# Kernel tuning notes

Measured on AMD Instinct MI355X. Metric: run time of the kernel, lower is better.

## Reference

```python
import jax, jax.numpy as jnp
import numpy as np

N, E = 50000, 400000
H, C = 2, 128          # heads, embedding_size
HC = H * C
HID = 256              # hidden_size
TARGET = 1234
NEG_SLOPE = 0.2


def gatv2_conv(x, src, dst, edge_attr, Wl, bl, Wr, br, We, att, b_out):
    """PyG GATv2Conv, concat=True, share_weights=False, edge_dim given."""
    n = x.shape[0]
    xl = (x @ Wl + bl).reshape(n, H, C)   # lin_l -> source side
    xr = (x @ Wr + br).reshape(n, H, C)   # lin_r -> target side
    e = (edge_attr @ We).reshape(-1, H, C)  # lin_edge (no bias)
    m = xl[src] + xr[dst] + e             # [E,H,C]
    s = jax.nn.leaky_relu(m, NEG_SLOPE)
    alpha = jnp.einsum('ehc,hc->eh', s, att)  # [E,H]
    # segment softmax over destination nodes
    amax = jax.ops.segment_max(alpha, dst, num_segments=n)
    amax = jnp.where(jnp.isfinite(amax), amax, 0.0)
    ex = jnp.exp(alpha - amax[dst])
    den = jax.ops.segment_sum(ex, dst, num_segments=n)
    a = ex / (den[dst] + 1e-16)
    msg = (xl[src] * a[:, :, None]).reshape(-1, HC)
    out = jax.ops.segment_sum(msg, dst, num_segments=n)
    return out + b_out                    # [N, H*C]


def setup_inputs() -> dict:
    key = jax.random.key(0)
    ks = jax.random.split(key, 20)
    g = lambda k, shp, s=0.1: (jax.random.normal(k, shp, dtype=jnp.float32) * s)
    inp = {
        'x': jax.random.normal(ks[0], (N, 2), dtype=jnp.float32),
        'edge_index': jax.random.randint(ks[1], (2, E), 0, N, dtype=jnp.int32),
        'edge_attr': jax.random.uniform(ks[2], (E, 1), dtype=jnp.float32),
        'labels': jnp.zeros((N,), dtype=jnp.int32).at[TARGET].set(1),
        # conv1 params (in=2)
        'Wl1': g(ks[3], (2, HC)), 'bl1': jnp.zeros((HC,), jnp.float32),
        'Wr1': g(ks[4], (2, HC)), 'br1': jnp.zeros((HC,), jnp.float32),
        'We1': g(ks[5], (1, HC)), 'att1': g(ks[6], (H, C)),
        'bo1': jnp.zeros((HC,), jnp.float32),
        # conv2 params (lazy in_channels inferred as 2, since it is fed x)
        'Wl2': g(ks[7], (2, HC)), 'bl2': jnp.zeros((HC,), jnp.float32),
        'Wr2': g(ks[8], (2, HC)), 'br2': jnp.zeros((HC,), jnp.float32),
        'We2': g(ks[9], (1, HC)), 'att2': g(ks[10], (H, C)),
        'bo2': jnp.zeros((HC,), jnp.float32),
        # fc
        'Wfc': g(ks[11], (HC, HID)), 'bfc': jnp.zeros((HID,), jnp.float32),
    }
    return inp


def reference(x, edge_index, edge_attr, labels,
              Wl1, bl1, Wr1, br1, We1, att1, bo1,
              Wl2, bl2, Wr2, br2, We2, att2, bo2,
              Wfc, bfc):
    src, dst = edge_index[0], edge_index[1]
    # conv1 (computed as in source; its output is overwritten by conv2(x))
    h1 = jax.nn.relu(gatv2_conv(x, src, dst, edge_attr, Wl1, bl1, Wr1, br1, We1, att1, bo1))
    h = jax.nn.relu(gatv2_conv(x, src, dst, edge_attr, Wl2, bl2, Wr2, br2, We2, att2, bo2))
    target_idx = jnp.argmax(labels)
    te = h[target_idx][None, :]           # [1, H*C]
    out = te @ Wfc + bfc                  # [1, hidden]
    return out
```

## Files before the change

kernel.cpp:

```cpp
#include <hip/hip_runtime.h>
#include <stdint.h>


#define MAXE 512
#define NEG_SLOPE 0.2f
#define HC 256
#define FCBLOCKS 8

struct Ws {
    unsigned long long key;
    int count;
    int pad;
    int list[MAXE];
};

__device__ __forceinline__ unsigned long long enc_key(int val, int idx) {
    return ((unsigned long long)(~(((unsigned)val) ^ 0x80000000u)) << 32)
           | (unsigned long long)(unsigned)idx;
}

__global__ void argmax_zero_kernel(const int* __restrict__ labels, int n,
                                   Ws* __restrict__ ws, float* __restrict__ out) {
    __shared__ unsigned long long sred[256];
    const int tid = threadIdx.x;
    int t = blockIdx.x * blockDim.x + tid;
    unsigned long long best = ~0ull;
    int i0 = t * 4;
    if (i0 + 3 < n) {
        int4 v = *reinterpret_cast<const int4*>(labels + i0);
        int vals[4] = {v.x, v.y, v.z, v.w};
        #pragma unroll
        for (int j = 0; j < 4; ++j) {
            unsigned long long key = enc_key(vals[j], i0 + j);
            if (key < best) best = key;
        }
    } else {
        for (int j = 0; j < 4; ++j) {
            int i = i0 + j;
            if (i < n) {
                unsigned long long key = enc_key(labels[i], i);
                if (key < best) best = key;
            }
        }
    }
    sred[tid] = best;
    __syncthreads();
    for (int off = 128; off > 0; off >>= 1) {
        if (tid < off) {
            if (sred[tid + off] < sred[tid]) sred[tid] = sred[tid + off];
        }
        __syncthreads();
    }
    if (tid == 0) atomicMin(&ws->key, sred[0]);
    if (blockIdx.x == 0) {
        if (tid == 0) ws->count = 0;
        out[tid] = 0.f;
    }
}

__device__ __forceinline__ int decode_target(const Ws* ws) {
    return (int)(unsigned)(ws->key & 0xFFFFFFFFull);
}

__global__ void filter_kernel(const int* __restrict__ dstArr, int E,
                              Ws* __restrict__ ws) {
    const int target = decode_target(ws);
    int t = blockIdx.x * blockDim.x + threadIdx.x;
    int i0 = t * 4;
    if (i0 + 3 < E) {
        int4 v = *reinterpret_cast<const int4*>(dstArr + i0);
        int vals[4] = {v.x, v.y, v.z, v.w};
        #pragma unroll
        for (int j = 0; j < 4; ++j) {
            if (vals[j] == target) {
                int pos = atomicAdd(&ws->count, 1);
                if (pos < MAXE) ws->list[pos] = i0 + j;
            }
        }
    } else {
        for (int j = 0; j < 4; ++j) {
            int i = i0 + j;
            if (i < E && dstArr[i] == target) {
                int pos = atomicAdd(&ws->count, 1);
                if (pos < MAXE) ws->list[pos] = i;
            }
        }
    }
}

__global__ void gat_fc_kernel(const float* __restrict__ x,
                              const int* __restrict__ srcArr,
                              const float* __restrict__ edge_attr,
                              const float* __restrict__ Wl, const float* __restrict__ bl,
                              const float* __restrict__ Wr, const float* __restrict__ br,
                              const float* __restrict__ We, const float* __restrict__ att,
                              const float* __restrict__ bo,
                              const float* __restrict__ Wfc, const float* __restrict__ bfc,
                              const Ws* __restrict__ ws,
                              float* __restrict__ out) {
    const int tid = threadIdx.x;
    const int h = tid >> 7;

    __shared__ float sx0[MAXE], sx1[MAXE], sea[MAXE];
    __shared__ float salpha[2 * MAXE];
    __shared__ float wred[4];
    __shared__ float te_s[HC];

    const int target = decode_target(ws);
    int K = ws->count;
    if (K > MAXE) K = MAXE;

    const float xt0 = x[2 * target], xt1 = x[2 * target + 1];
    const float wl0 = Wl[tid], wl1 = Wl[HC + tid], blv = bl[tid];
    const float xr  = xt0 * Wr[tid] + xt1 * Wr[HC + tid] + br[tid];
    const float wev = We[tid];
    const float attv = att[tid];

    for (int base = 0; base < K; base += 256) {
        int k = base + tid;
        if (k < K) {
            int e = ws->list[k];
            int s = srcArr[e];
            sx0[k] = x[2 * s];
            sx1[k] = x[2 * s + 1];
            sea[k] = edge_attr[e];
        }
    }
    __syncthreads();

    for (int k = 0; k < K; ++k) {
        float xl = sx0[k] * wl0 + sx1[k] * wl1 + blv;
        float m = xl + xr + sea[k] * wev;
        float sl = (m >= 0.f) ? m : NEG_SLOPE * m;
        float v = sl * attv;
        #pragma unroll
        for (int off = 32; off > 0; off >>= 1) v += __shfl_down(v, off, 64);
        if ((tid & 63) == 0) wred[tid >> 6] = v;
        __syncthreads();
        if (tid == 0) {
            salpha[2 * k]     = wred[0] + wred[1];
            salpha[2 * k + 1] = wred[2] + wred[3];
        }
        __syncthreads();
    }

    float amax = -3.0e38f;
    for (int k = 0; k < K; ++k) amax = fmaxf(amax, salpha[2 * k + h]);
    float den = 0.f;
    for (int k = 0; k < K; ++k) den += expf(salpha[2 * k + h] - amax);
    float inv = 1.f / (den + 1e-16f);

    float msg = 0.f;
    for (int k = 0; k < K; ++k) {
        float xl = sx0[k] * wl0 + sx1[k] * wl1 + blv;
        msg += expf(salpha[2 * k + h] - amax) * inv * xl;
    }
    float tv = msg + bo[tid];
    te_s[tid] = tv > 0.f ? tv : 0.f;
    __syncthreads();

    float acc = (blockIdx.x == 0) ? bfc[tid] : 0.f;
    const int r0 = blockIdx.x * (HC / FCBLOCKS);
    #pragma unroll
    for (int r = 0; r < HC / FCBLOCKS; ++r)
        acc += te_s[r0 + r] * Wfc[(r0 + r) * HC + tid];
    atomicAdd(&out[tid], acc);
}

extern "C" void kernel_launch(void* const* d_in, const int* in_sizes, int n_in,
                              void* d_out, int out_size, void* d_ws, size_t ws_size,
                              hipStream_t stream) {
    const float* x          = (const float*)d_in[0];
    const int*   edge_index = (const int*)  d_in[1];
    const float* edge_attr  = (const float*)d_in[2];
    const int*   labels     = (const int*)  d_in[3];
    const float* Wl2  = (const float*)d_in[11];
    const float* bl2  = (const float*)d_in[12];
    const float* Wr2  = (const float*)d_in[13];
    const float* br2  = (const float*)d_in[14];
    const float* We2  = (const float*)d_in[15];
    const float* att2 = (const float*)d_in[16];
    const float* bo2  = (const float*)d_in[17];
    const float* Wfc  = (const float*)d_in[18];
    const float* bfc  = (const float*)d_in[19];

    const int N = in_sizes[3];
    const int E = in_sizes[1] / 2;
    const int* srcArr = edge_index;
    const int* dstArr = edge_index + E;

    Ws* ws = (Ws*)d_ws;
    float* out = (float*)d_out;

    int n4 = (N + 3) / 4;
    argmax_zero_kernel<<<(n4 + 255) / 256, 256, 0, stream>>>(labels, N, ws, out);

    int e4 = (E + 3) / 4;
    filter_kernel<<<(e4 + 255) / 256, 256, 0, stream>>>(dstArr, E, ws);

    gat_fc_kernel<<<FCBLOCKS, 256, 0, stream>>>(x, srcArr, edge_attr,
                                                Wl2, bl2, Wr2, br2, We2, att2, bo2,
                                                Wfc, bfc, ws, out);
}
```

Baseline: 102.8 us.

## Fuse argmax, edge filter and GAT/FC into one persistent kernel with grid barriers

Replaces the three launches (label argmax, destination-edge filter, attention plus FC) with a single 96-block kernel. Stages are separated by atomic-counter grid barriers with spin-sleep. Each thread prefetches its dst int4 chunks before waiting on the first barrier, and the FC weight rows are loaded into registers early to hide latency. The first barrier assumes the workspace counter starts at a fixed poison value, and the spin barriers assume all blocks are co-resident.

```diff
diff --git a/kernel.cpp b/kernel.cpp
--- a/kernel.cpp
+++ b/kernel.cpp
@@ -2,13 +2,19 @@
 #include <stdint.h>
 
 
+#define GRID 96
+#define FCB  32
+#define ROWS (256 / FCB)
 #define MAXE 512
 #define NEG_SLOPE 0.2f
 #define HC 256
-#define FCBLOCKS 8
+#define EPT 8
+#define POIS32 0xAAAAAAAAu
 
 struct Ws {
     unsigned long long key;
+    unsigned int done1;
+    unsigned int done2;
     int count;
     int pad;
     int list[MAXE];
@@ -19,112 +25,146 @@
            | (unsigned long long)(unsigned)idx;
 }
 
-__global__ void argmax_zero_kernel(const int* __restrict__ labels, int n,
-                                   Ws* __restrict__ ws, float* __restrict__ out) {
+__global__ void __launch_bounds__(256) fused_kernel(
+    const float* __restrict__ x,
+    const int* __restrict__ srcArr, const int* __restrict__ dstArr,
+    const float* __restrict__ edge_attr, const int* __restrict__ labels,
+    int N, int E,
+    const float* __restrict__ Wl, const float* __restrict__ bl,
+    const float* __restrict__ Wr, const float* __restrict__ br,
+    const float* __restrict__ We, const float* __restrict__ att,
+    const float* __restrict__ bo,
+    const float* __restrict__ Wfc, const float* __restrict__ bfc,
+    Ws* __restrict__ ws, float* __restrict__ out)
+{
+    const int tid = threadIdx.x;
+    const int blk = blockIdx.x;
+    const int g   = blk * 256 + tid;
+    const int T   = GRID * 256;
+    const int h   = tid >> 7;
+
     __shared__ unsigned long long sred[256];
-    const int tid = threadIdx.x;
-    int t = blockIdx.x * blockDim.x + tid;
-    unsigned long long best = ~0ull;
-    int i0 = t * 4;
-    if (i0 + 3 < n) {
-        int4 v = *reinterpret_cast<const int4*>(labels + i0);
-        int vals[4] = {v.x, v.y, v.z, v.w};
-        #pragma unroll
-        for (int j = 0; j < 4; ++j) {
-            unsigned long long key = enc_key(vals[j], i0 + j);
-            if (key < best) best = key;
-        }
-    } else {
-        for (int j = 0; j < 4; ++j) {
-            int i = i0 + j;
-            if (i < n) {
-                unsigned long long key = enc_key(labels[i], i);
-                if (key < best) best = key;
-            }
-        }
-    }
-    sred[tid] = best;
-    __syncthreads();
-    for (int off = 128; off > 0; off >>= 1) {
-        if (tid < off) {
-            if (sred[tid + off] < sred[tid]) sred[tid] = sred[tid + off];
-        }
-        __syncthreads();
-    }
-    if (tid == 0) atomicMin(&ws->key, sred[0]);
-    if (blockIdx.x == 0) {
-        if (tid == 0) ws->count = 0;
-        out[tid] = 0.f;
-    }
-}
-
-__device__ __forceinline__ int decode_target(const Ws* ws) {
-    return (int)(unsigned)(ws->key & 0xFFFFFFFFull);
-}
-
-__global__ void filter_kernel(const int* __restrict__ dstArr, int E,
-                              Ws* __restrict__ ws) {
-    const int target = decode_target(ws);
-    int t = blockIdx.x * blockDim.x + threadIdx.x;
-    int i0 = t * 4;
-    if (i0 + 3 < E) {
-        int4 v = *reinterpret_cast<const int4*>(dstArr + i0);
-        int vals[4] = {v.x, v.y, v.z, v.w};
-        #pragma unroll
-        for (int j = 0; j < 4; ++j) {
-            if (vals[j] == target) {
-                int pos = atomicAdd(&ws->count, 1);
-                if (pos < MAXE) ws->list[pos] = i0 + j;
-            }
-        }
-    } else {
-        for (int j = 0; j < 4; ++j) {
-            int i = i0 + j;
-            if (i < E && dstArr[i] == target) {
-                int pos = atomicAdd(&ws->count, 1);
-                if (pos < MAXE) ws->list[pos] = i;
-            }
-        }
-    }
-}
-
-__global__ void gat_fc_kernel(const float* __restrict__ x,
-                              const int* __restrict__ srcArr,
-                              const float* __restrict__ edge_attr,
-                              const float* __restrict__ Wl, const float* __restrict__ bl,
-                              const float* __restrict__ Wr, const float* __restrict__ br,
-                              const float* __restrict__ We, const float* __restrict__ att,
-                              const float* __restrict__ bo,
-                              const float* __restrict__ Wfc, const float* __restrict__ bfc,
-                              const Ws* __restrict__ ws,
-                              float* __restrict__ out) {
-    const int tid = threadIdx.x;
-    const int h = tid >> 7;
-
     __shared__ float sx0[MAXE], sx1[MAXE], sea[MAXE];
     __shared__ float salpha[2 * MAXE];
     __shared__ float wred[4];
     __shared__ float te_s[HC];
 
-    const int target = decode_target(ws);
-    int K = ws->count;
+    float wfc_r[ROWS];
+    float wl0 = 0.f, wl1 = 0.f, blv = 0.f, wr0 = 0.f, wr1 = 0.f, brv = 0.f;
+    float wev = 0.f, attv = 0.f, bov = 0.f, bfcv = 0.f;
+    if (blk < FCB) {
+        const int r0 = blk * ROWS;
+        #pragma unroll
+        for (int r = 0; r < ROWS; ++r) wfc_r[r] = Wfc[(r0 + r) * HC + tid];
+        wl0 = Wl[tid]; wl1 = Wl[HC + tid]; blv = bl[tid];
+        wr0 = Wr[tid]; wr1 = Wr[HC + tid]; brv = br[tid];
+        wev = We[tid]; attv = att[tid]; bov = bo[tid];
+        bfcv = (blk == 0) ? bfc[tid] : 0.f;
+    }
+
+    unsigned long long best = ~0ull;
+    const int NI4 = N >> 2;
+    for (int i4 = g; i4 < NI4; i4 += T) {
+        int4 v = *reinterpret_cast<const int4*>(labels + (size_t)i4 * 4);
+        int vals[4] = {v.x, v.y, v.z, v.w};
+        #pragma unroll
+        for (int j = 0; j < 4; ++j) {
+            unsigned long long key = enc_key(vals[j], i4 * 4 + j);
+            if (key < best) best = key;
+        }
+    }
+    if (g == 0) {
+        for (int i = NI4 * 4; i < N; ++i) {
+            unsigned long long key = enc_key(labels[i], i);
+            if (key < best) best = key;
+        }
+    }
+    sred[tid] = best;
+    __syncthreads();
+    for (int off = 128; off > 0; off >>= 1) {
+        if (tid < off) { if (sred[tid + off] < sred[tid]) sred[tid] = sred[tid + off]; }
+        __syncthreads();
+    }
+    if (blk == 0) {
+        out[tid] = 0.f;
+        if (tid == 0) { ws->count = 0; ws->done2 = 0u; }
+    }
+    __threadfence();
+    __syncthreads();
+    if (tid == 0) {
+        atomicMin(&ws->key, sred[0]);
+        __threadfence();
+        atomicAdd(&ws->done1, 1u);
+    }
+
+    int4 dv[EPT];
+    bool dok[EPT];
+    const int EI4 = E >> 2;
+    #pragma unroll
+    for (int j = 0; j < EPT; ++j) {
+        int i4 = g + j * T;
+        dok[j] = (i4 < EI4);
+        if (dok[j]) dv[j] = *reinterpret_cast<const int4*>(dstArr + (size_t)i4 * 4);
+    }
+
+    if (tid == 0) {
+        while (__hip_atomic_load(&ws->done1, __ATOMIC_RELAXED, __HIP_MEMORY_SCOPE_AGENT)
+               != POIS32 + (unsigned)GRID)
+            __builtin_amdgcn_s_sleep(2);
+    }
+    __syncthreads();
+    __threadfence();
+
+    const unsigned long long kv =
+        __hip_atomic_load(&ws->key, __ATOMIC_RELAXED, __HIP_MEMORY_SCOPE_AGENT);
+    const int target = (int)(unsigned)(kv & 0xFFFFFFFFull);
+
+    #pragma unroll
+    for (int j = 0; j < EPT; ++j) {
+        if (dok[j]) {
+            int base = (g + j * T) * 4;
+            int vals[4] = {dv[j].x, dv[j].y, dv[j].z, dv[j].w};
+            #pragma unroll
+            for (int q = 0; q < 4; ++q) {
+                if (vals[q] == target) {
+                    int pos = atomicAdd(&ws->count, 1);
+                    if (pos < MAXE) ws->list[pos] = base + q;
+                }
+            }
+        }
+    }
+    if (g == 0) {
+        for (int i = EI4 * 4; i < E; ++i) {
+            if (dstArr[i] == target) {
+                int pos = atomicAdd(&ws->count, 1);
+                if (pos < MAXE) ws->list[pos] = i;
+            }
+        }
+    }
+    __threadfence();
+    __syncthreads();
+    if (tid == 0) atomicAdd(&ws->done2, 1u);
+    if (blk >= FCB) return;
+
+    if (tid == 0) {
+        while (__hip_atomic_load(&ws->done2, __ATOMIC_RELAXED, __HIP_MEMORY_SCOPE_AGENT)
+               != (unsigned)GRID)
+            __builtin_amdgcn_s_sleep(2);
+    }
+    __syncthreads();
+    __threadfence();
+
+    int K = __hip_atomic_load(&ws->count, __ATOMIC_RELAXED, __HIP_MEMORY_SCOPE_AGENT);
     if (K > MAXE) K = MAXE;
 
-    const float xt0 = x[2 * target], xt1 = x[2 * target + 1];
-    const float wl0 = Wl[tid], wl1 = Wl[HC + tid], blv = bl[tid];
-    const float xr  = xt0 * Wr[tid] + xt1 * Wr[HC + tid] + br[tid];
-    const float wev = We[tid];
-    const float attv = att[tid];
-
-    for (int base = 0; base < K; base += 256) {
-        int k = base + tid;
-        if (k < K) {
-            int e = ws->list[k];
-            int s = srcArr[e];
-            sx0[k] = x[2 * s];
-            sx1[k] = x[2 * s + 1];
-            sea[k] = edge_attr[e];
-        }
+    const float2 xt = *reinterpret_cast<const float2*>(x + 2 * (size_t)target);
+    const float xr = xt.x * wr0 + xt.y * wr1 + brv;
+
+    for (int k = tid; k < K; k += 256) {
+        int e = ws->list[k];
+        int s = srcArr[e];
+        float2 xs = *reinterpret_cast<const float2*>(x + 2 * (size_t)s);
+        sx0[k] = xs.x; sx1[k] = xs.y; sea[k] = edge_attr[e];
     }
     __syncthreads();
 
@@ -155,15 +195,14 @@
         float xl = sx0[k] * wl0 + sx1[k] * wl1 + blv;
         msg += expf(salpha[2 * k + h] - amax) * inv * xl;
     }
-    float tv = msg + bo[tid];
+    float tv = msg + bov;
     te_s[tid] = tv > 0.f ? tv : 0.f;
     __syncthreads();
 
-    float acc = (blockIdx.x == 0) ? bfc[tid] : 0.f;
-    const int r0 = blockIdx.x * (HC / FCBLOCKS);
+    float acc = bfcv;
+    const int r0 = blk * ROWS;
     #pragma unroll
-    for (int r = 0; r < HC / FCBLOCKS; ++r)
-        acc += te_s[r0 + r] * Wfc[(r0 + r) * HC + tid];
+    for (int r = 0; r < ROWS; ++r) acc += te_s[r0 + r] * wfc_r[r];
     atomicAdd(&out[tid], acc);
 }
 
@@ -192,13 +231,8 @@
     Ws* ws = (Ws*)d_ws;
     float* out = (float*)d_out;
 
-    int n4 = (N + 3) / 4;
-    argmax_zero_kernel<<<(n4 + 255) / 256, 256, 0, stream>>>(labels, N, ws, out);
-
-    int e4 = (E + 3) / 4;
-    filter_kernel<<<(e4 + 255) / 256, 256, 0, stream>>>(dstArr, E, ws);
-
-    gat_fc_kernel<<<FCBLOCKS, 256, 0, stream>>>(x, srcArr, edge_attr,
-                                                Wl2, bl2, Wr2, br2, We2, att2, bo2,
-                                                Wfc, bfc, ws, out);
+    fused_kernel<<<GRID, 256, 0, stream>>>(x, srcArr, dstArr, edge_attr, labels,
+                                           N, E,
+                                           Wl2, bl2, Wr2, br2, We2, att2, bo2,
+                                           Wfc, bfc, ws, out);
 }
```

Measured after the change: 124.6 us. +21.2%, slower.
